# Performance work log

Hardware: AMD Instinct MI355X
Metric: run time of the kernel (lower is better)

## Reference

```python
import jax, jax.numpy as jnp
import numpy as np

B, S, D, H, DH = 2, 2048, 768, 12, 64
ROT, BASE, WIN = 64, 10000.0, 128
SCALE = float(np.sqrt(DH))  # cfg.attn_scale = sqrt(d_head) = 8.0


def _sin_cos():
    # TransformerLens calculate_sin_cos_rotary, rotary_adjacent_pairs=False
    pos = jnp.arange(S, dtype=jnp.float32)
    freq = BASE ** (jnp.arange(0, ROT, 2, dtype=jnp.float32) / ROT)
    freq = jnp.concatenate([freq, freq])  # 'd -> (2 d)'
    angles = pos[:, None] / freq[None, :]  # [S, ROT]
    return jnp.sin(angles), jnp.cos(angles)


def _rotate_every_two(v):
    n = v.shape[-1] // 2
    return jnp.concatenate([-v[..., n:], v[..., :n]], axis=-1)


def _apply_rotary(x, sin, cos):
    # x: [B, S, H, DH]; rotate first ROT dims, pass rest through
    xr, xp = x[..., :ROT], x[..., ROT:]
    c = cos[None, :, None, :]
    s = sin[None, :, None, :]
    return jnp.concatenate([xr * c + _rotate_every_two(xr) * s, xp], axis=-1)


def setup_inputs() -> dict:
    key = jax.random.key(0)
    ks = jax.random.split(key, 7)
    init = lambda k, shape: jax.random.normal(k, shape, jnp.float32) / np.sqrt(D).astype(np.float32)
    return dict(
        query_input=jax.random.normal(ks[0], (B, S, D), jnp.float32),
        key_input=jax.random.normal(ks[1], (B, S, D), jnp.float32),
        value_input=jax.random.normal(ks[2], (B, S, D), jnp.float32),
        W_Q=init(ks[3], (H, D, DH)),
        W_K=init(ks[4], (H, D, DH)),
        W_V=init(ks[5], (H, D, DH)),
        W_O=init(ks[6], (H, DH, D)),
        b_Q=jnp.zeros((H, DH), jnp.float32),
        b_K=jnp.zeros((H, DH), jnp.float32),
        b_V=jnp.zeros((H, DH), jnp.float32),
        b_O=jnp.zeros((D,), jnp.float32),
    )


def reference(query_input, key_input, value_input, W_Q, W_K, W_V, W_O, b_Q, b_K, b_V, b_O):
    # QKV projections (calculate_qkv_matrices)
    q = jnp.einsum('bpd,hdk->bphk', query_input, W_Q) + b_Q
    k = jnp.einsum('bpd,hdk->bphk', key_input, W_K) + b_K
    v = jnp.einsum('bpd,hdk->bphk', value_input, W_V) + b_V
    # rotary (kv_cache_pos_offset = 0)
    sin, cos = _sin_cos()
    q = _apply_rotary(q, sin, cos)
    k = _apply_rotary(k, sin, cos)
    # attention scores
    scores = jnp.einsum('bqhd,bkhd->bhqk', q, k) / SCALE
    # position_bias defaults to zeros -> no-op
    i = jnp.arange(S)[:, None]
    j = jnp.arange(S)[None, :]
    mask = (j <= i) & (j > i - WIN)
    scores = jnp.where(mask[None, None], scores, -jnp.inf)
    pattern = jax.nn.softmax(scores, axis=-1)
    pattern = jnp.where(jnp.isnan(pattern), 0.0, pattern)
    z = jnp.einsum('bhqk,bkhd->bqhd', pattern, v)  # [B, S, H, DH]
    # output projection: z flattened @ W_O (rearranged) + b_O
    out = z.reshape(B, S, H * DH) @ W_O.reshape(H * DH, D) + b_O
    return out
```

## Files before the change

### kernel.cpp

```cpp
#include <hip/hip_runtime.h>
#include <hip/hip_bf16.h>

#define BB 2
#define SS 2048
#define DD 768
#define HH 12
#define DHH 64
#define WIN 128
#define MM (BB*SS)

typedef __attribute__((ext_vector_type(8))) short bfrag;
typedef __attribute__((ext_vector_type(4))) float f32x4;

#define AS3(p) ((__attribute__((address_space(3))) void*)(p))
#define AS1(p) ((const __attribute__((address_space(1))) void*)(p))

__device__ inline unsigned short f2bf(float f) {
    union { __hip_bfloat16 h; unsigned short u; } cv;
    cv.h = __float2bfloat16(f);
    return cv.u;
}

__global__ __launch_bounds__(256) void pack_kernel(
    const float* __restrict__ Wq, const float* __restrict__ Wk, const float* __restrict__ Wv,
    const float* __restrict__ Wo,
    unsigned short* __restrict__ Wt, unsigned short* __restrict__ Wot,
    float2* __restrict__ rope)
{
    __shared__ float T[64][65];
    const int bid = blockIdx.x, t = threadIdx.x;
    if (bid < 432) {
        int proj = bid / 144, rem = bid % 144;
        int h = rem / 12, d0 = (rem % 12) * 64;
        const float* src = (proj == 0 ? Wq : (proj == 1 ? Wk : Wv)) + (size_t)h * DD * DHH;
        int row = t >> 2, c0 = (t & 3) * 16;
        const float4* p4 = reinterpret_cast<const float4*>(src + (size_t)(d0 + row) * DHH + c0);
        float4 x0 = p4[0], x1 = p4[1], x2 = p4[2], x3 = p4[3];
        float* tr = &T[row][c0];
        tr[0]=x0.x; tr[1]=x0.y; tr[2]=x0.z; tr[3]=x0.w;
        tr[4]=x1.x; tr[5]=x1.y; tr[6]=x1.z; tr[7]=x1.w;
        tr[8]=x2.x; tr[9]=x2.y; tr[10]=x2.z; tr[11]=x2.w;
        tr[12]=x3.x; tr[13]=x3.y; tr[14]=x3.z; tr[15]=x3.w;
        __syncthreads();
        int dh = t >> 2;
        unsigned short tmp[16];
        #pragma unroll
        for (int j = 0; j < 16; j++) tmp[j] = f2bf(T[c0 + j][dh]);
        unsigned short* dst = Wt + (size_t)proj * DD * DD + (size_t)(h * 64 + dh) * DD + d0 + c0;
        *reinterpret_cast<bfrag*>(dst)     = *reinterpret_cast<bfrag*>(tmp);
        *reinterpret_cast<bfrag*>(dst + 8) = *reinterpret_cast<bfrag*>(tmp + 8);
    } else if (bid < 576) {
        int id2 = bid - 432;
        int k0 = (id2 / 12) * 64, n0 = (id2 % 12) * 64;
        int row = t >> 2, c0 = (t & 3) * 16;
        const float4* p4 = reinterpret_cast<const float4*>(Wo + (size_t)(k0 + row) * DD + n0 + c0);
        float4 x0 = p4[0], x1 = p4[1], x2 = p4[2], x3 = p4[3];
        float* tr = &T[row][c0];
        tr[0]=x0.x; tr[1]=x0.y; tr[2]=x0.z; tr[3]=x0.w;
        tr[4]=x1.x; tr[5]=x1.y; tr[6]=x1.z; tr[7]=x1.w;
        tr[8]=x2.x; tr[9]=x2.y; tr[10]=x2.z; tr[11]=x2.w;
        tr[12]=x3.x; tr[13]=x3.y; tr[14]=x3.z; tr[15]=x3.w;
        __syncthreads();
        int nr = t >> 2;
        unsigned short tmp[16];
        #pragma unroll
        for (int j = 0; j < 16; j++) tmp[j] = f2bf(T[c0 + j][nr]);
        unsigned short* dst = Wot + (size_t)(n0 + nr) * DD + k0 + c0;
        *reinterpret_cast<bfrag*>(dst)     = *reinterpret_cast<bfrag*>(tmp);
        *reinterpret_cast<bfrag*>(dst + 8) = *reinterpret_cast<bfrag*>(tmp + 8);
    } else {
        int idx = (bid - 576) * 256 + t;
        int p = idx >> 5, i2 = idx & 31;
        float inv_freq = exp2f(-(float)i2 * (13.287712379549449f / 32.0f));
        float s, c;
        sincosf((float)p * inv_freq, &s, &c);
        rope[idx] = make_float2(s, c);
    }
}

__global__ __launch_bounds__(256) void qkv_gemm_kernel(
    const float* __restrict__ Xq, const float* __restrict__ Xk, const float* __restrict__ Xv,
    const unsigned short* __restrict__ Wt,
    const float* __restrict__ bq, const float* __restrict__ bk, const float* __restrict__ bv,
    const float2* __restrict__ rope,
    unsigned short* __restrict__ qo, unsigned short* __restrict__ ko, unsigned short* __restrict__ vo)
{
    const int mt0  = blockIdx.x * 128;
    const int n0   = blockIdx.y * 128;
    const int proj = blockIdx.z;
    const float* X = proj == 0 ? Xq : (proj == 1 ? Xk : Xv);
    const unsigned short* W = Wt + (size_t)proj * DD * DD;
    const float* bias = proj == 0 ? bq : (proj == 1 ? bk : bv);

    __shared__ unsigned short smem[128 * 140];
    unsigned short* As = smem;
    unsigned short* Bs = smem + 4096;

    const int t = threadIdx.x;
    const int l = t & 63, w4 = t >> 6;
    const int l16 = l & 15, quad = l >> 4;
    const int wr = w4 >> 1, wc = w4 & 1;
    const int swz = (l16 >> 1) & 3;

    f32x4 acc[16] = {};

    const int arow = t >> 1, ac0 = (t & 1) * 16;
    const int as_ = (arow >> 1) & 3;
    const int ak8 = ac0 >> 3;
    const float* Xrow = X + (size_t)(mt0 + arow) * DD + ac0;

    for (int k0 = 0; k0 < DD; k0 += 32) {
        #pragma unroll
        for (int j = 0; j < 2; j++) {
            int eoff = (w4 * 2 + j) * 512;
            int e = eoff + l * 8;
            int row = e >> 5, cs = (e & 31) >> 3;
            int k8 = cs ^ ((row >> 1) & 3);
            __builtin_amdgcn_global_load_lds(
                AS1(W + (size_t)(n0 + row) * DD + k0 + k8 * 8),
                AS3(Bs + eoff), 16, 0, 0);
        }
        {
            const float4* p4 = reinterpret_cast<const float4*>(Xrow + k0);
            float4 a0 = p4[0], a1 = p4[1], a2 = p4[2], a3 = p4[3];
            unsigned short u[16];
            u[0]=f2bf(a0.x); u[1]=f2bf(a0.y); u[2]=f2bf(a0.z); u[3]=f2bf(a0.w);
            u[4]=f2bf(a1.x); u[5]=f2bf(a1.y); u[6]=f2bf(a1.z); u[7]=f2bf(a1.w);
            u[8]=f2bf(a2.x); u[9]=f2bf(a2.y); u[10]=f2bf(a2.z); u[11]=f2bf(a2.w);
            u[12]=f2bf(a3.x); u[13]=f2bf(a3.y); u[14]=f2bf(a3.z); u[15]=f2bf(a3.w);
            *reinterpret_cast<bfrag*>(&As[arow * 32 + ((ak8 ^ as_) * 8)])       = *reinterpret_cast<bfrag*>(u);
            *reinterpret_cast<bfrag*>(&As[arow * 32 + (((ak8 + 1) ^ as_) * 8)]) = *reinterpret_cast<bfrag*>(u + 8);
        }
        __syncthreads();
        bfrag af[4], bg[4];
        #pragma unroll
        for (int mi = 0; mi < 4; mi++)
            af[mi] = *reinterpret_cast<const bfrag*>(&As[(wr * 64 + mi * 16 + l16) * 32 + ((quad ^ swz) * 8)]);
        #pragma unroll
        for (int ni = 0; ni < 4; ni++)
            bg[ni] = *reinterpret_cast<const bfrag*>(&Bs[(wc * 64 + ni * 16 + l16) * 32 + ((quad ^ swz) * 8)]);
        #pragma unroll
        for (int mi = 0; mi < 4; mi++)
            #pragma unroll
            for (int ni = 0; ni < 4; ni++)
                acc[mi * 4 + ni] = __builtin_amdgcn_mfma_f32_16x16x32_bf16(af[mi], bg[ni], acc[mi * 4 + ni], 0, 0, 0);
        __syncthreads();
    }

    unsigned short* Ct = smem;
    const int b = mt0 >> 11;
    if (proj < 2) {
        #pragma unroll
        for (int ni = 0; ni < 4; ni++) {
            int nloc = wc * 64 + ni * 16 + l16;
            int n = n0 + nloc;
            int dh = n & 63;
            float bv0 = bias[n];
            float bv1 = bias[n ^ 32];
            float sgn = (dh & 32) ? 1.0f : -1.0f;
            const float2* rp = rope + (dh & 31);
            #pragma unroll
            for (int mi = 0; mi < 4; mi++)
                #pragma unroll
                for (int r = 0; r < 4; r++) {
                    int ploc = wr * 64 + mi * 16 + quad * 4 + r;
                    int p = (mt0 + ploc) & (SS - 1);
                    float2 sc = rp[p << 5];
                    float val = acc[mi * 4 + ni][r] + bv0;
                    float pr  = acc[mi * 4 + (ni ^ 2)][r] + bv1;
                    Ct[ploc * 140 + nloc] = f2bf(val * sc.y + sgn * pr * sc.x);
                }
        }
        __syncthreads();
        unsigned short* dst = (proj == 0) ? qo : ko;
        #pragma unroll
        for (int jj = 0; jj < 8; jj++) {
            int id = jj * 256 + t;
            int row = id >> 4, c = (id & 15) * 8;
            int n = n0 + c, h = n >> 6, dh = n & 63;
            int p = (mt0 + row) & (SS - 1);
            bfrag vv = *reinterpret_cast<const bfrag*>(&Ct[row * 140 + c]);
            *reinterpret_cast<bfrag*>(dst + (((size_t)(b * HH + h) * SS + p) << 6) + dh) = vv;
        }
    } else {
        #pragma unroll
        for (int ni = 0; ni < 4; ni++) {
            int nloc = wc * 64 + ni * 16 + l16;
            float bv0 = bias[n0 + nloc];
            #pragma unroll
            for (int mi = 0; mi < 4; mi++)
                #pragma unroll
                for (int r = 0; r < 4; r++) {
                    int ploc = wr * 64 + mi * 16 + quad * 4 + r;
                    Ct[nloc * 140 + ploc] = f2bf(acc[mi * 4 + ni][r] + bv0);
                }
        }
        __syncthreads();
        int p0 = mt0 & (SS - 1);
        #pragma unroll
        for (int jj = 0; jj < 8; jj++) {
            int id = jj * 256 + t;
            int row = id >> 4, c = (id & 15) * 8;
            int n = n0 + row, h = n >> 6, dh = n & 63;
            bfrag vv = *reinterpret_cast<const bfrag*>(&Ct[row * 140 + c]);
            *reinterpret_cast<bfrag*>(vo + (((size_t)(b * HH + h) * DHH + dh) << 11) + p0 + c) = vv;
        }
    }
}

__global__ __launch_bounds__(256) void attn_kernel(
    const unsigned short* __restrict__ q,
    const unsigned short* __restrict__ k,
    const unsigned short* __restrict__ v,
    unsigned short* __restrict__ z)
{
    const int qb = blockIdx.x * 64;
    const int h  = blockIdx.y;
    const int b  = blockIdx.z;
    const int kb = qb - WIN;

    __shared__ unsigned short QK[64 * 72 + 192 * 72];
    __shared__ unsigned short Ps[64 * 200];
    unsigned short* Qs = QK;
    unsigned short* Ks = QK + 64 * 72;
    unsigned short* Vt = QK;

    const int t = threadIdx.x;
    const int w = t >> 6, lane = t & 63;
    const int l16 = lane & 15, quad = lane >> 4;

    const size_t qkbase = ((size_t)(b * HH + h) * SS) * DHH;
    #pragma unroll
    for (int i = 0; i < 2; i++) {
        int chunk = i * 256 + t;
        int row = chunk >> 3, c0 = (chunk & 7) * 8;
        bfrag val = *reinterpret_cast<const bfrag*>(q + qkbase + (size_t)(qb + row) * DHH + c0);
        *reinterpret_cast<bfrag*>(&Qs[row * 72 + c0]) = val;
    }
    #pragma unroll
    for (int i = 0; i < 6; i++) {
        int chunk = i * 256 + t;
        int row = chunk >> 3, c0 = (chunk & 7) * 8;
        int src = kb + row; if (src < 0) src = 0;
        bfrag val = *reinterpret_cast<const bfrag*>(k + qkbase + (size_t)src * DHH + c0);
        *reinterpret_cast<bfrag*>(&Ks[row * 72 + c0]) = val;
    }
    __syncthreads();

    f32x4 sacc[12] = {};
    #pragma unroll
    for (int kk = 0; kk < 64; kk += 32) {
        bfrag a = *reinterpret_cast<const bfrag*>(&Qs[(16 * w + l16) * 72 + kk + quad * 8]);
        #pragma unroll
        for (int mt = 0; mt < 12; mt++) {
            bfrag bf = *reinterpret_cast<const bfrag*>(&Ks[(16 * mt + l16) * 72 + kk + quad * 8]);
            sacc[mt] = __builtin_amdgcn_mfma_f32_16x16x32_bf16(a, bf, sacc[mt], 0, 0, 0);
        }
    }

    float mx[4] = {-3e38f, -3e38f, -3e38f, -3e38f};
    #pragma unroll
    for (int mt = 0; mt < 12; mt++)
        #pragma unroll
        for (int r = 0; r < 4; r++) {
            int row = 16 * w + quad * 4 + r;
            int c = 16 * mt + l16;
            bool valid = (c > row) && (c <= row + WIN) && (kb + c >= 0);
            float s = valid ? sacc[mt][r] * 0.125f : -3e38f;
            sacc[mt][r] = s;
            mx[r] = fmaxf(mx[r], s);
        }
    #pragma unroll
    for (int off = 1; off < 16; off <<= 1)
        #pragma unroll
        for (int r = 0; r < 4; r++) mx[r] = fmaxf(mx[r], __shfl_xor(mx[r], off, 64));
    float sum[4] = {0.f, 0.f, 0.f, 0.f};
    #pragma unroll
    for (int mt = 0; mt < 12; mt++)
        #pragma unroll
        for (int r = 0; r < 4; r++) {
            float p = __expf(sacc[mt][r] - mx[r]);
            sacc[mt][r] = p;
            sum[r] += p;
        }
    #pragma unroll
    for (int off = 1; off < 16; off <<= 1)
        #pragma unroll
        for (int r = 0; r < 4; r++) sum[r] += __shfl_xor(sum[r], off, 64);
    float inv[4];
    #pragma unroll
    for (int r = 0; r < 4; r++) inv[r] = 1.0f / sum[r];

    #pragma unroll
    for (int mt = 0; mt < 12; mt++)
        #pragma unroll
        for (int r = 0; r < 4; r++)
            Ps[(16 * w + quad * 4 + r) * 200 + 16 * mt + l16] = f2bf(sacc[mt][r] * inv[r]);
    __syncthreads();

    const size_t vbase = ((size_t)(b * HH + h) * DHH) * SS;
    if (kb >= 0) {
        #pragma unroll
        for (int i = 0; i < 6; i++) {
            int chunk = i * 256 + t;
            int d = chunk / 24, c0 = (chunk % 24) * 8;
            bfrag val = *reinterpret_cast<const bfrag*>(v + vbase + (size_t)d * SS + kb + c0);
            *reinterpret_cast<bfrag*>(&Vt[d * 200 + c0]) = val;
        }
    } else {
        for (int i = 0; i < 6; i++) {
            int chunk = i * 256 + t;
            int d = chunk / 24, c0 = (chunk % 24) * 8;
            unsigned short tmp[8];
            for (int j2 = 0; j2 < 8; j2++) {
                int src = kb + c0 + j2; if (src < 0) src = 0;
                tmp[j2] = v[vbase + (size_t)d * SS + src];
            }
            for (int j2 = 0; j2 < 8; j2++) Vt[d * 200 + c0 + j2] = tmp[j2];
        }
    }
    __syncthreads();

    f32x4 zacc[4] = {};
    #pragma unroll
    for (int c0 = 0; c0 < 192; c0 += 32) {
        bfrag a = *reinterpret_cast<const bfrag*>(&Ps[(16 * w + l16) * 200 + c0 + quad * 8]);
        #pragma unroll
        for (int nt = 0; nt < 4; nt++) {
            bfrag bf = *reinterpret_cast<const bfrag*>(&Vt[(16 * nt + l16) * 200 + c0 + quad * 8]);
            zacc[nt] = __builtin_amdgcn_mfma_f32_16x16x32_bf16(a, bf, zacc[nt], 0, 0, 0);
        }
    }
    #pragma unroll
    for (int nt = 0; nt < 4; nt++)
        #pragma unroll
        for (int r = 0; r < 4; r++) {
            int row = 16 * w + quad * 4 + r;
            int d = 16 * nt + l16;
            z[((size_t)(b * SS + qb + row)) * (HH * DHH) + h * DHH + d] = f2bf(zacc[nt][r]);
        }
}

__global__ __launch_bounds__(256) void out_gemm_kernel(
    const unsigned short* __restrict__ Z,
    const unsigned short* __restrict__ Wot,
    const float* __restrict__ bo,
    float* __restrict__ out)
{
    const int mt0 = blockIdx.x * 128;
    const int n0  = blockIdx.y * 128;

    __shared__ unsigned short smem[8192];
    unsigned short* As = smem;
    unsigned short* Bs = smem + 4096;

    const int t = threadIdx.x;
    const int l = t & 63, w4 = t >> 6;
    const int l16 = l & 15, quad = l >> 4;
    const int wr = w4 >> 1, wc = w4 & 1;
    const int swz = (l16 >> 1) & 3;

    f32x4 acc[16] = {};

    for (int k0 = 0; k0 < DD; k0 += 32) {
        #pragma unroll
        for (int j = 0; j < 2; j++) {
            int eoff = (w4 * 2 + j) * 512;
            int e = eoff + l * 8;
            int row = e >> 5, cs = (e & 31) >> 3;
            int k8 = cs ^ ((row >> 1) & 3);
            __builtin_amdgcn_global_load_lds(
                AS1(Z + (size_t)(mt0 + row) * DD + k0 + k8 * 8),
                AS3(As + eoff), 16, 0, 0);
            __builtin_amdgcn_global_load_lds(
                AS1(Wot + (size_t)(n0 + row) * DD + k0 + k8 * 8),
                AS3(Bs + eoff), 16, 0, 0);
        }
        __syncthreads();
        bfrag af[4], bg[4];
        #pragma unroll
        for (int mi = 0; mi < 4; mi++)
            af[mi] = *reinterpret_cast<const bfrag*>(&As[(wr * 64 + mi * 16 + l16) * 32 + ((quad ^ swz) * 8)]);
        #pragma unroll
        for (int ni = 0; ni < 4; ni++)
            bg[ni] = *reinterpret_cast<const bfrag*>(&Bs[(wc * 64 + ni * 16 + l16) * 32 + ((quad ^ swz) * 8)]);
        #pragma unroll
        for (int mi = 0; mi < 4; mi++)
            #pragma unroll
            for (int ni = 0; ni < 4; ni++)
                acc[mi * 4 + ni] = __builtin_amdgcn_mfma_f32_16x16x32_bf16(af[mi], bg[ni], acc[mi * 4 + ni], 0, 0, 0);
        __syncthreads();
    }

    #pragma unroll
    for (int ni = 0; ni < 4; ni++) {
        int n = n0 + wc * 64 + ni * 16 + l16;
        float bv0 = bo[n];
        #pragma unroll
        for (int mi = 0; mi < 4; mi++)
            #pragma unroll
            for (int r = 0; r < 4; r++) {
                int m = mt0 + wr * 64 + mi * 16 + quad * 4 + r;
                out[(size_t)m * DD + n] = acc[mi * 4 + ni][r] + bv0;
            }
    }
}

extern "C" void kernel_launch(void* const* d_in, const int* in_sizes, int n_in,
                              void* d_out, int out_size, void* d_ws, size_t ws_size,
                              hipStream_t stream) {
    const float* Xq = (const float*)d_in[0];
    const float* Xk = (const float*)d_in[1];
    const float* Xv = (const float*)d_in[2];
    const float* Wq = (const float*)d_in[3];
    const float* Wk = (const float*)d_in[4];
    const float* Wv = (const float*)d_in[5];
    const float* Wo = (const float*)d_in[6];
    const float* bq = (const float*)d_in[7];
    const float* bk = (const float*)d_in[8];
    const float* bv = (const float*)d_in[9];
    const float* bo = (const float*)d_in[10];
    float* out = (float*)d_out;

    const size_t seg = (size_t)BB * HH * SS * DHH;
    unsigned short* q   = (unsigned short*)d_ws;
    unsigned short* k   = q + seg;
    unsigned short* v   = k + seg;
    unsigned short* z   = v + seg;
    unsigned short* Wt  = z + seg;
    unsigned short* Wot = Wt + (size_t)3 * DD * DD;
    float2* rope = (float2*)(Wot + (size_t)DD * DD);

    pack_kernel<<<dim3(832), 256, 0, stream>>>(Wq, Wk, Wv, Wo, Wt, Wot, rope);
    qkv_gemm_kernel<<<dim3(MM / 128, DD / 128, 3), 256, 0, stream>>>(
        Xq, Xk, Xv, Wt, bq, bk, bv, rope, q, k, v);
    attn_kernel<<<dim3(SS / 64, HH, BB), 256, 0, stream>>>(q, k, v, z);
    out_gemm_kernel<<<dim3(MM / 128, DD / 128), 256, 0, stream>>>(z, Wot, bo, out);
}
```

Before: 189.7 us.

## Pre-convert inputs to bf16, double-buffer GEMM LDS loads, shrink out-GEMM tiles

The pack kernel now also converts the fp32 Q/K/V activations to bf16 in a workspace buffer, so the QKV GEMM can stage both operands with async global_load_lds instead of doing register loads and conversions inside its loop. Both GEMMs now use double-buffered LDS with one barrier per k-step, so the next tile loads while the current one is computed. The output GEMM tile is cut from 128x128 to 64x128 to launch more blocks. In exchange, the activations make an extra round trip through memory as bf16, and the pack kernel has more blocks to run.

```diff
diff --git a/kernel.cpp b/kernel.cpp
--- a/kernel.cpp
+++ b/kernel.cpp
@@ -21,11 +21,34 @@
     return cv.u;
 }
 
+__device__ inline void stage128(unsigned short* dst, const unsigned short* src,
+                                int w4, int l) {
+    #pragma unroll
+    for (int j = 0; j < 2; j++) {
+        int eoff = (w4 * 2 + j) * 512;
+        int e = eoff + l * 8;
+        int row = e >> 5;
+        int k8 = ((e >> 3) & 3) ^ ((row >> 1) & 3);
+        __builtin_amdgcn_global_load_lds(AS1(src + (size_t)row * DD + k8 * 8),
+                                         AS3(dst + eoff), 16, 0, 0);
+    }
+}
+__device__ inline void stage64(unsigned short* dst, const unsigned short* src,
+                               int w4, int l) {
+    int eoff = w4 * 512;
+    int e = eoff + l * 8;
+    int row = e >> 5;
+    int k8 = ((e >> 3) & 3) ^ ((row >> 1) & 3);
+    __builtin_amdgcn_global_load_lds(AS1(src + (size_t)row * DD + k8 * 8),
+                                     AS3(dst + eoff), 16, 0, 0);
+}
+
 __global__ __launch_bounds__(256) void pack_kernel(
+    const float* __restrict__ Xq, const float* __restrict__ Xk, const float* __restrict__ Xv,
     const float* __restrict__ Wq, const float* __restrict__ Wk, const float* __restrict__ Wv,
     const float* __restrict__ Wo,
     unsigned short* __restrict__ Wt, unsigned short* __restrict__ Wot,
-    float2* __restrict__ rope)
+    float2* __restrict__ rope, unsigned short* __restrict__ Xbf)
 {
     __shared__ float T[64][65];
     const int bid = blockIdx.x, t = threadIdx.x;
@@ -68,18 +91,33 @@
         unsigned short* dst = Wot + (size_t)(n0 + nr) * DD + k0 + c0;
         *reinterpret_cast<bfrag*>(dst)     = *reinterpret_cast<bfrag*>(tmp);
         *reinterpret_cast<bfrag*>(dst + 8) = *reinterpret_cast<bfrag*>(tmp + 8);
-    } else {
+    } else if (bid < 832) {
         int idx = (bid - 576) * 256 + t;
         int p = idx >> 5, i2 = idx & 31;
         float inv_freq = exp2f(-(float)i2 * (13.287712379549449f / 32.0f));
         float s, c;
         sincosf((float)p * inv_freq, &s, &c);
         rope[idx] = make_float2(s, c);
+    } else {
+        int i = bid - 832;
+        int proj = i / 768;
+        size_t off = (size_t)(i % 768) * 4096 + t * 16;
+        const float* src = (proj == 0 ? Xq : (proj == 1 ? Xk : Xv)) + off;
+        const float4* p4 = reinterpret_cast<const float4*>(src);
+        float4 a0 = p4[0], a1 = p4[1], a2 = p4[2], a3 = p4[3];
+        unsigned short u[16];
+        u[0]=f2bf(a0.x); u[1]=f2bf(a0.y); u[2]=f2bf(a0.z); u[3]=f2bf(a0.w);
+        u[4]=f2bf(a1.x); u[5]=f2bf(a1.y); u[6]=f2bf(a1.z); u[7]=f2bf(a1.w);
+        u[8]=f2bf(a2.x); u[9]=f2bf(a2.y); u[10]=f2bf(a2.z); u[11]=f2bf(a2.w);
+        u[12]=f2bf(a3.x); u[13]=f2bf(a3.y); u[14]=f2bf(a3.z); u[15]=f2bf(a3.w);
+        unsigned short* dst = Xbf + (size_t)proj * MM * DD + off;
+        *reinterpret_cast<bfrag*>(dst)     = *reinterpret_cast<bfrag*>(u);
+        *reinterpret_cast<bfrag*>(dst + 8) = *reinterpret_cast<bfrag*>(u + 8);
     }
 }
 
 __global__ __launch_bounds__(256) void qkv_gemm_kernel(
-    const float* __restrict__ Xq, const float* __restrict__ Xk, const float* __restrict__ Xv,
+    const unsigned short* __restrict__ Xbf,
     const unsigned short* __restrict__ Wt,
     const float* __restrict__ bq, const float* __restrict__ bk, const float* __restrict__ bv,
     const float2* __restrict__ rope,
@@ -88,13 +126,11 @@
     const int mt0  = blockIdx.x * 128;
     const int n0   = blockIdx.y * 128;
     const int proj = blockIdx.z;
-    const float* X = proj == 0 ? Xq : (proj == 1 ? Xk : Xv);
-    const unsigned short* W = Wt + (size_t)proj * DD * DD;
+    const unsigned short* X = Xbf + (size_t)proj * MM * DD + (size_t)mt0 * DD;
+    const unsigned short* W = Wt + (size_t)proj * DD * DD + (size_t)n0 * DD;
     const float* bias = proj == 0 ? bq : (proj == 1 ? bk : bv);
 
     __shared__ unsigned short smem[128 * 140];
-    unsigned short* As = smem;
-    unsigned short* Bs = smem + 4096;
 
     const int t = threadIdx.x;
     const int l = t & 63, w4 = t >> 6;
@@ -104,48 +140,32 @@
 
     f32x4 acc[16] = {};
 
-    const int arow = t >> 1, ac0 = (t & 1) * 16;
-    const int as_ = (arow >> 1) & 3;
-    const int ak8 = ac0 >> 3;
-    const float* Xrow = X + (size_t)(mt0 + arow) * DD + ac0;
-
-    for (int k0 = 0; k0 < DD; k0 += 32) {
-        #pragma unroll
-        for (int j = 0; j < 2; j++) {
-            int eoff = (w4 * 2 + j) * 512;
-            int e = eoff + l * 8;
-            int row = e >> 5, cs = (e & 31) >> 3;
-            int k8 = cs ^ ((row >> 1) & 3);
-            __builtin_amdgcn_global_load_lds(
-                AS1(W + (size_t)(n0 + row) * DD + k0 + k8 * 8),
-                AS3(Bs + eoff), 16, 0, 0);
-        }
-        {
-            const float4* p4 = reinterpret_cast<const float4*>(Xrow + k0);
-            float4 a0 = p4[0], a1 = p4[1], a2 = p4[2], a3 = p4[3];
-            unsigned short u[16];
-            u[0]=f2bf(a0.x); u[1]=f2bf(a0.y); u[2]=f2bf(a0.z); u[3]=f2bf(a0.w);
-            u[4]=f2bf(a1.x); u[5]=f2bf(a1.y); u[6]=f2bf(a1.z); u[7]=f2bf(a1.w);
-            u[8]=f2bf(a2.x); u[9]=f2bf(a2.y); u[10]=f2bf(a2.z); u[11]=f2bf(a2.w);
-            u[12]=f2bf(a3.x); u[13]=f2bf(a3.y); u[14]=f2bf(a3.z); u[15]=f2bf(a3.w);
-            *reinterpret_cast<bfrag*>(&As[arow * 32 + ((ak8 ^ as_) * 8)])       = *reinterpret_cast<bfrag*>(u);
-            *reinterpret_cast<bfrag*>(&As[arow * 32 + (((ak8 + 1) ^ as_) * 8)]) = *reinterpret_cast<bfrag*>(u + 8);
-        }
-        __syncthreads();
+    stage128(smem,        X, w4, l);
+    stage128(smem + 4096, W, w4, l);
+
+    for (int it = 0; it < 24; ++it) {
+        unsigned short* Ac = smem + (it & 1) * 8192;
+        unsigned short* Bc = Ac + 4096;
+        __syncthreads();
+        if (it < 23) {
+            unsigned short* An = smem + ((it + 1) & 1) * 8192;
+            stage128(An,        X + (it + 1) * 32, w4, l);
+            stage128(An + 4096, W + (it + 1) * 32, w4, l);
+        }
         bfrag af[4], bg[4];
         #pragma unroll
         for (int mi = 0; mi < 4; mi++)
-            af[mi] = *reinterpret_cast<const bfrag*>(&As[(wr * 64 + mi * 16 + l16) * 32 + ((quad ^ swz) * 8)]);
+            af[mi] = *reinterpret_cast<const bfrag*>(&Ac[(wr * 64 + mi * 16 + l16) * 32 + ((quad ^ swz) * 8)]);
         #pragma unroll
         for (int ni = 0; ni < 4; ni++)
-            bg[ni] = *reinterpret_cast<const bfrag*>(&Bs[(wc * 64 + ni * 16 + l16) * 32 + ((quad ^ swz) * 8)]);
+            bg[ni] = *reinterpret_cast<const bfrag*>(&Bc[(wc * 64 + ni * 16 + l16) * 32 + ((quad ^ swz) * 8)]);
         #pragma unroll
         for (int mi = 0; mi < 4; mi++)
             #pragma unroll
             for (int ni = 0; ni < 4; ni++)
                 acc[mi * 4 + ni] = __builtin_amdgcn_mfma_f32_16x16x32_bf16(af[mi], bg[ni], acc[mi * 4 + ni], 0, 0, 0);
-        __syncthreads();
-    }
+    }
+    __syncthreads();
 
     unsigned short* Ct = smem;
     const int b = mt0 >> 11;
@@ -347,61 +367,56 @@
     const float* __restrict__ bo,
     float* __restrict__ out)
 {
-    const int mt0 = blockIdx.x * 128;
+    const int mt0 = blockIdx.x * 64;
     const int n0  = blockIdx.y * 128;
-
-    __shared__ unsigned short smem[8192];
-    unsigned short* As = smem;
-    unsigned short* Bs = smem + 4096;
+    const unsigned short* A = Z + (size_t)mt0 * DD;
+    const unsigned short* Bw = Wot + (size_t)n0 * DD;
+
+    __shared__ unsigned short smem[12288];
 
     const int t = threadIdx.x;
     const int l = t & 63, w4 = t >> 6;
     const int l16 = l & 15, quad = l >> 4;
-    const int wr = w4 >> 1, wc = w4 & 1;
     const int swz = (l16 >> 1) & 3;
 
-    f32x4 acc[16] = {};
-
-    for (int k0 = 0; k0 < DD; k0 += 32) {
-        #pragma unroll
-        for (int j = 0; j < 2; j++) {
-            int eoff = (w4 * 2 + j) * 512;
-            int e = eoff + l * 8;
-            int row = e >> 5, cs = (e & 31) >> 3;
-            int k8 = cs ^ ((row >> 1) & 3);
-            __builtin_amdgcn_global_load_lds(
-                AS1(Z + (size_t)(mt0 + row) * DD + k0 + k8 * 8),
-                AS3(As + eoff), 16, 0, 0);
-            __builtin_amdgcn_global_load_lds(
-                AS1(Wot + (size_t)(n0 + row) * DD + k0 + k8 * 8),
-                AS3(Bs + eoff), 16, 0, 0);
-        }
-        __syncthreads();
-        bfrag af[4], bg[4];
+    f32x4 acc[8] = {};
+
+    stage64 (smem,        A,  w4, l);
+    stage128(smem + 2048, Bw, w4, l);
+
+    for (int it = 0; it < 24; ++it) {
+        unsigned short* Ac = smem + (it & 1) * 6144;
+        unsigned short* Bc = Ac + 2048;
+        __syncthreads();
+        if (it < 23) {
+            unsigned short* An = smem + ((it + 1) & 1) * 6144;
+            stage64 (An,        A  + (it + 1) * 32, w4, l);
+            stage128(An + 2048, Bw + (it + 1) * 32, w4, l);
+        }
+        bfrag af[4], bg[2];
         #pragma unroll
         for (int mi = 0; mi < 4; mi++)
-            af[mi] = *reinterpret_cast<const bfrag*>(&As[(wr * 64 + mi * 16 + l16) * 32 + ((quad ^ swz) * 8)]);
-        #pragma unroll
-        for (int ni = 0; ni < 4; ni++)
-            bg[ni] = *reinterpret_cast<const bfrag*>(&Bs[(wc * 64 + ni * 16 + l16) * 32 + ((quad ^ swz) * 8)]);
+            af[mi] = *reinterpret_cast<const bfrag*>(&Ac[(mi * 16 + l16) * 32 + ((quad ^ swz) * 8)]);
+        #pragma unroll
+        for (int ni = 0; ni < 2; ni++)
+            bg[ni] = *reinterpret_cast<const bfrag*>(&Bc[(w4 * 32 + ni * 16 + l16) * 32 + ((quad ^ swz) * 8)]);
         #pragma unroll
         for (int mi = 0; mi < 4; mi++)
             #pragma unroll
-            for (int ni = 0; ni < 4; ni++)
-                acc[mi * 4 + ni] = __builtin_amdgcn_mfma_f32_16x16x32_bf16(af[mi], bg[ni], acc[mi * 4 + ni], 0, 0, 0);
-        __syncthreads();
-    }
-
-    #pragma unroll
-    for (int ni = 0; ni < 4; ni++) {
-        int n = n0 + wc * 64 + ni * 16 + l16;
+            for (int ni = 0; ni < 2; ni++)
+                acc[mi * 2 + ni] = __builtin_amdgcn_mfma_f32_16x16x32_bf16(af[mi], bg[ni], acc[mi * 2 + ni], 0, 0, 0);
+    }
+
+    #pragma unroll
+    for (int ni = 0; ni < 2; ni++) {
+        int n = n0 + w4 * 32 + ni * 16 + l16;
         float bv0 = bo[n];
         #pragma unroll
         for (int mi = 0; mi < 4; mi++)
             #pragma unroll
             for (int r = 0; r < 4; r++) {
-                int m = mt0 + wr * 64 + mi * 16 + quad * 4 + r;
-                out[(size_t)m * DD + n] = acc[mi * 4 + ni][r] + bv0;
+                int m = mt0 + mi * 16 + quad * 4 + r;
+                out[(size_t)m * DD + n] = acc[mi * 2 + ni][r] + bv0;
             }
     }
 }
@@ -430,10 +445,11 @@
     unsigned short* Wt  = z + seg;
     unsigned short* Wot = Wt + (size_t)3 * DD * DD;
     float2* rope = (float2*)(Wot + (size_t)DD * DD);
-
-    pack_kernel<<<dim3(832), 256, 0, stream>>>(Wq, Wk, Wv, Wo, Wt, Wot, rope);
+    unsigned short* Xbf = (unsigned short*)(rope + 2048 * 32);
+
+    pack_kernel<<<dim3(3136), 256, 0, stream>>>(Xq, Xk, Xv, Wq, Wk, Wv, Wo, Wt, Wot, rope, Xbf);
     qkv_gemm_kernel<<<dim3(MM / 128, DD / 128, 3), 256, 0, stream>>>(
-        Xq, Xk, Xv, Wt, bq, bk, bv, rope, q, k, v);
+        Xbf, Wt, bq, bk, bv, rope, q, k, v);
     attn_kernel<<<dim3(SS / 64, HH, BB), 256, 0, stream>>>(q, k, v, z);
-    out_gemm_kernel<<<dim3(MM / 128, DD / 128), 256, 0, stream>>>(z, Wot, bo, out);
-}
+    out_gemm_kernel<<<dim3(MM / 64, DD / 128), 256, 0, stream>>>(z, Wot, bo, out);
+}
```

Measured after the change: 169.1 us. -10.9%, faster.
